# Performance work log

Hardware: AMD Instinct MI355X
Metric: run time of the kernel (lower is better)

## Reference

```python
import jax, jax.numpy as jnp
import numpy as np

B, N, F_IN, F_OUT = 4, 2048, 128, 128

def setup_inputs() -> dict:
    key = jax.random.key(0)
    k1, k2, k3, k4 = jax.random.split(key, 4)
    node_features = jax.random.uniform(k1, (B, N, F_IN), dtype=jnp.float32)
    adjacency = jax.random.uniform(k2, (B, N, N), dtype=jnp.float32)
    # nn.Linear(in_dim, out_dim) params
    lim = 1.0 / np.sqrt(F_IN)
    W = jax.random.uniform(k3, (F_OUT, F_IN), minval=-lim, maxval=lim, dtype=jnp.float32)
    b = jax.random.uniform(k4, (F_OUT,), minval=-lim, maxval=lim, dtype=jnp.float32)
    return {"node_features": node_features, "adjacency": adjacency, "W": W, "b": b}

def reference(node_features, adjacency, W, b):
    # degree_inv_sqrt, same math as diag_embed matmuls but via row/col scaling
    degree = adjacency.sum(axis=-1)                              # [B, N]
    d_inv_sqrt = jnp.clip(degree, 1e-6, None) ** -0.5            # [B, N]
    norm_adj = adjacency * d_inv_sqrt[:, :, None] * d_inv_sqrt[:, None, :]  # [B, N, N]
    agg = jnp.einsum('bnm,bmf->bnf', norm_adj, node_features)    # [B, N, F_in]
    return agg @ W.T + b                                         # [B, N, F_out]
```

## Files before the change

### kernel.cpp

```cpp
#include <hip/hip_runtime.h>


#define NN 2048
#define FF 128
#define WS_NEED (32768u + 4u * 128u * 2048u * 2u)

typedef __attribute__((ext_vector_type(4))) float f32x4;
typedef __attribute__((ext_vector_type(8))) short short8;

__device__ inline float bf2f(unsigned short h) {
    return __builtin_bit_cast(float, ((unsigned)h) << 16);
}
__device__ inline unsigned short f2bf(float f) {
    unsigned u = __builtin_bit_cast(unsigned, f);
    u = (u + 0x7fffu + ((u >> 16) & 1u)) >> 16;
    return (unsigned short)u;
}

__device__ inline short8 cvt8(f32x4 a, f32x4 b) {
    short8 r;
    r[0] = (short)f2bf(a.x); r[1] = (short)f2bf(a.y);
    r[2] = (short)f2bf(a.z); r[3] = (short)f2bf(a.w);
    r[4] = (short)f2bf(b.x); r[5] = (short)f2bf(b.y);
    r[6] = (short)f2bf(b.z); r[7] = (short)f2bf(b.w);
    return r;
}

__global__ __launch_bounds__(256) void k1_deg(const float* __restrict__ A,
                                              float* __restrict__ dinv) {
    __shared__ float red[256];
    int row = blockIdx.x;
    int t = threadIdx.x;
    const f32x4* ap = (const f32x4*)(A + (size_t)row * NN);
    f32x4 v0 = ap[t];
    f32x4 v1 = ap[t + 256];
    red[t] = v0.x + v0.y + v0.z + v0.w + v1.x + v1.y + v1.z + v1.w;
    __syncthreads();
    #pragma unroll
    for (int s = 128; s > 0; s >>= 1) {
        if (t < s) red[t] += red[t + s];
        __syncthreads();
    }
    if (t == 0) dinv[row] = rsqrtf(fmaxf(red[0], 1e-6f));
}

__global__ __launch_bounds__(256) void k2_zt(const float* __restrict__ X,
                                             const float* __restrict__ W,
                                             const float* __restrict__ dinv,
                                             unsigned short* __restrict__ Zt) {
    __shared__ float Ws[FF * FF];
    int blk = blockIdx.x;
    int b  = blk >> 6;
    int mc = (blk >> 3) & 7;
    int oc = blk & 7;
    int t  = threadIdx.x;
    int m  = mc * 256 + t;

    {
        f32x4* wd = (f32x4*)Ws;
        const f32x4* wsrc = (const f32x4*)W;
        #pragma unroll
        for (int j = 0; j < 16; ++j) wd[t + 256 * j] = wsrc[t + 256 * j];
    }
    __syncthreads();

    float acc[16];
    #pragma unroll
    for (int j = 0; j < 16; ++j) acc[j] = 0.f;

    const f32x4* xr = (const f32x4*)(X + ((size_t)b * NN + m) * FF);
    for (int f4 = 0; f4 < FF / 4; ++f4) {
        f32x4 xv = xr[f4];
        #pragma unroll
        for (int j = 0; j < 16; ++j) {
            f32x4 wv = *(const f32x4*)&Ws[(oc * 16 + j) * FF + f4 * 4];
            acc[j] += xv.x * wv.x + xv.y * wv.y + xv.z * wv.z + xv.w * wv.w;
        }
    }
    float dv = dinv[b * NN + m];
    #pragma unroll
    for (int j = 0; j < 16; ++j)
        Zt[((size_t)b * FF + oc * 16 + j) * NN + m] = f2bf(acc[j] * dv);
}

__global__ __launch_bounds__(256) void k3_mfma(const float* __restrict__ A,
                                               const unsigned short* __restrict__ Zt,
                                               const float* __restrict__ dinv,
                                               const float* __restrict__ bias,
                                               float* __restrict__ out) {
    __shared__ unsigned short As[2][16][72];
    __shared__ unsigned short Zs[2][128][72];
    int blk = blockIdx.x;
    int b   = blk >> 7;
    int n0  = (blk & 127) * 16;
    int t   = threadIdx.x;
    int w   = t >> 6, lane = t & 63;
    int l15 = lane & 15, kgrp = (lane >> 4) * 8;

    const float* Ab = A + (size_t)b * NN * NN;
    const unsigned short* Zb = Zt + (size_t)b * FF * NN;

    int ar = t >> 3;
    int ac = (t & 7) * 8;
    int zo = t >> 1;
    int zk = (t & 1) * 32;

    f32x4 acc[2];
    acc[0] = (f32x4){0.f, 0.f, 0.f, 0.f};
    acc[1] = (f32x4){0.f, 0.f, 0.f, 0.f};

    f32x4 pa0, pa1;  short8 pz0, pz1, pz2, pz3;
    f32x4 qa0, qa1;  short8 qz0, qz1, qz2, qz3;

    #define LOADT(A0, A1, Z0, Z1, Z2, Z3, k0)                                \
        do {                                                                 \
            if (t < 128) {                                                   \
                const float* asrc = Ab + (size_t)(n0 + ar) * NN + (k0) + ac; \
                A0 = *(const f32x4*)asrc;                                    \
                A1 = *(const f32x4*)(asrc + 4);                              \
            }                                                                \
            const unsigned short* zsrc = Zb + (size_t)zo * NN + (k0) + zk;   \
            Z0 = *(const short8*)(zsrc);                                     \
            Z1 = *(const short8*)(zsrc + 8);                                 \
            Z2 = *(const short8*)(zsrc + 16);                                \
            Z3 = *(const short8*)(zsrc + 24);                                \
        } while (0)

    #define WRITET(buf, A0, A1, Z0, Z1, Z2, Z3)                              \
        do {                                                                 \
            if (t < 128) *(short8*)&As[buf][ar][ac] = cvt8(A0, A1);          \
            *(short8*)&Zs[buf][zo][zk]      = Z0;                            \
            *(short8*)&Zs[buf][zo][zk + 8]  = Z1;                            \
            *(short8*)&Zs[buf][zo][zk + 16] = Z2;                            \
            *(short8*)&Zs[buf][zo][zk + 24] = Z3;                            \
        } while (0)

    #define MFMAS(cur)                                                       \
        do {                                                                 \
            _Pragma("unroll")                                                \
            for (int ks = 0; ks < 64; ks += 32) {                            \
                short8 af = *(const short8*)&As[cur][l15][ks + kgrp];        \
                short8 bf0 = *(const short8*)&Zs[cur][w * 32 + l15][ks + kgrp];       \
                short8 bf1 = *(const short8*)&Zs[cur][w * 32 + 16 + l15][ks + kgrp];  \
                acc[0] = __builtin_amdgcn_mfma_f32_16x16x32_bf16(af, bf0, acc[0], 0, 0, 0); \
                acc[1] = __builtin_amdgcn_mfma_f32_16x16x32_bf16(af, bf1, acc[1], 0, 0, 0); \
            }                                                                \
        } while (0)

    LOADT(pa0, pa1, pz0, pz1, pz2, pz3, 0);
    WRITET(0, pa0, pa1, pz0, pz1, pz2, pz3);
    LOADT(pa0, pa1, pz0, pz1, pz2, pz3, 64);
    __syncthreads();

    for (int it = 0; it < 32; it += 2) {
        if (it + 2 < 32) LOADT(qa0, qa1, qz0, qz1, qz2, qz3, (it + 2) * 64);
        MFMAS(0);
        if (it + 1 < 32) WRITET(1, pa0, pa1, pz0, pz1, pz2, pz3);
        __syncthreads();
        if (it + 1 < 32) {
            if (it + 3 < 32) LOADT(pa0, pa1, pz0, pz1, pz2, pz3, (it + 3) * 64);
            MFMAS(1);
            if (it + 2 < 32) WRITET(0, qa0, qa1, qz0, qz1, qz2, qz3);
            __syncthreads();
        }
    }

    int drow = (lane >> 4) * 4;
    #pragma unroll
    for (int tt = 0; tt < 2; ++tt) {
        int o = w * 32 + tt * 16 + l15;
        float bv = bias[o];
        #pragma unroll
        for (int r = 0; r < 4; ++r) {
            int n = n0 + drow + r;
            float dv = dinv[b * NN + n];
            out[((size_t)b * NN + n) * FF + o] = dv * acc[tt][r] + bv;
        }
    }
    #undef LOADT
    #undef WRITET
    #undef MFMAS
}

extern "C" void kernel_launch(void* const* d_in, const int* in_sizes, int n_in,
                              void* d_out, int out_size, void* d_ws, size_t ws_size,
                              hipStream_t stream) {
    const float *X = nullptr, *A = nullptr, *W = nullptr, *bias = nullptr;
    for (int i = 0; i < n_in; ++i) {
        switch (in_sizes[i]) {
            case 16777216: A    = (const float*)d_in[i]; break;
            case 1048576:  X    = (const float*)d_in[i]; break;
            case 16384:    W    = (const float*)d_in[i]; break;
            case 128:      bias = (const float*)d_in[i]; break;
            default: break;
        }
    }
    float* out = (float*)d_out;
    if (!X || !A || !W || !bias) return;
    if (out_size != 4 * NN * FF) return;
    if (ws_size < (size_t)WS_NEED) return;

    float* dinv        = (float*)d_ws;
    unsigned short* Zt = (unsigned short*)((char*)d_ws + 32768);

    k1_deg<<<4 * NN, 256, 0, stream>>>(A, dinv);
    k2_zt<<<256, 256, 0, stream>>>(X, W, dinv, Zt);
    k3_mfma<<<512, 256, 0, stream>>>(A, Zt, dinv, bias, out);
}
```

Measured before the change: 52.23 us.

## Retile aggregation kernel to 32x64 output tiles with 128-wide K steps

The MFMA aggregation kernel now assigns each block 32 node rows by 64 output features, instead of 16 rows by all 128 features, and arranges the four waves as a 2x2 grid of tiles. The K step grows from 64 to 128, which halves the number of loop iterations and barriers. All threads now load the adjacency tile, where before only half did. Each block reads half as much of the Z operand per output row, but every adjacency row is now read by two blocks, so the kernel relies on L2 to absorb that duplicate traffic on the largest tensor.

```diff
diff --git a/kernel.cpp b/kernel.cpp
--- a/kernel.cpp
+++ b/kernel.cpp
@@ -8,9 +8,6 @@
 typedef __attribute__((ext_vector_type(4))) float f32x4;
 typedef __attribute__((ext_vector_type(8))) short short8;
 
-__device__ inline float bf2f(unsigned short h) {
-    return __builtin_bit_cast(float, ((unsigned)h) << 16);
-}
 __device__ inline unsigned short f2bf(float f) {
     unsigned u = __builtin_bit_cast(unsigned, f);
     u = (u + 0x7fffu + ((u >> 16) & 1u)) >> 16;
@@ -88,79 +85,84 @@
                                                const float* __restrict__ dinv,
                                                const float* __restrict__ bias,
                                                float* __restrict__ out) {
-    __shared__ unsigned short As[2][16][72];
-    __shared__ unsigned short Zs[2][128][72];
+    __shared__ unsigned short As[2][32][136];
+    __shared__ unsigned short Zs[2][64][136];
     int blk = blockIdx.x;
     int b   = blk >> 7;
-    int n0  = (blk & 127) * 16;
+    int rem = blk & 127;
+    int n0  = (rem >> 1) * 32;
+    int o0  = (rem & 1) * 64;
     int t   = threadIdx.x;
     int w   = t >> 6, lane = t & 63;
+    int wr  = (w >> 1) * 16;
+    int wc  = (w & 1) * 32;
     int l15 = lane & 15, kgrp = (lane >> 4) * 8;
 
     const float* Ab = A + (size_t)b * NN * NN;
     const unsigned short* Zb = Zt + (size_t)b * FF * NN;
 
     int ar = t >> 3;
-    int ac = (t & 7) * 8;
-    int zo = t >> 1;
-    int zk = (t & 1) * 32;
+    int ac = (t & 7) * 16;
+    int zo = t >> 2;
+    int zc = (t & 3) * 32;
 
     f32x4 acc[2];
     acc[0] = (f32x4){0.f, 0.f, 0.f, 0.f};
     acc[1] = (f32x4){0.f, 0.f, 0.f, 0.f};
 
-    f32x4 pa0, pa1;  short8 pz0, pz1, pz2, pz3;
-    f32x4 qa0, qa1;  short8 qz0, qz1, qz2, qz3;
-
-    #define LOADT(A0, A1, Z0, Z1, Z2, Z3, k0)                                \
+    f32x4 pa0, pa1, pa2, pa3;  short8 pz0, pz1, pz2, pz3;
+    f32x4 qa0, qa1, qa2, qa3;  short8 qz0, qz1, qz2, qz3;
+
+    #define LOADT(A0, A1, A2, A3, Z0, Z1, Z2, Z3, k0)                        \
         do {                                                                 \
-            if (t < 128) {                                                   \
-                const float* asrc = Ab + (size_t)(n0 + ar) * NN + (k0) + ac; \
-                A0 = *(const f32x4*)asrc;                                    \
-                A1 = *(const f32x4*)(asrc + 4);                              \
-            }                                                                \
-            const unsigned short* zsrc = Zb + (size_t)zo * NN + (k0) + zk;   \
+            const float* asrc = Ab + (size_t)(n0 + ar) * NN + (k0) + ac;     \
+            A0 = *(const f32x4*)(asrc);                                      \
+            A1 = *(const f32x4*)(asrc + 4);                                  \
+            A2 = *(const f32x4*)(asrc + 8);                                  \
+            A3 = *(const f32x4*)(asrc + 12);                                 \
+            const unsigned short* zsrc = Zb + (size_t)(o0 + zo) * NN + (k0) + zc; \
             Z0 = *(const short8*)(zsrc);                                     \
             Z1 = *(const short8*)(zsrc + 8);                                 \
             Z2 = *(const short8*)(zsrc + 16);                                \
             Z3 = *(const short8*)(zsrc + 24);                                \
         } while (0)
 
-    #define WRITET(buf, A0, A1, Z0, Z1, Z2, Z3)                              \
+    #define WRITET(buf, A0, A1, A2, A3, Z0, Z1, Z2, Z3)                      \
         do {                                                                 \
-            if (t < 128) *(short8*)&As[buf][ar][ac] = cvt8(A0, A1);          \
-            *(short8*)&Zs[buf][zo][zk]      = Z0;                            \
-            *(short8*)&Zs[buf][zo][zk + 8]  = Z1;                            \
-            *(short8*)&Zs[buf][zo][zk + 16] = Z2;                            \
-            *(short8*)&Zs[buf][zo][zk + 24] = Z3;                            \
+            *(short8*)&As[buf][ar][ac]     = cvt8(A0, A1);                   \
+            *(short8*)&As[buf][ar][ac + 8] = cvt8(A2, A3);                   \
+            *(short8*)&Zs[buf][zo][zc]      = Z0;                            \
+            *(short8*)&Zs[buf][zo][zc + 8]  = Z1;                            \
+            *(short8*)&Zs[buf][zo][zc + 16] = Z2;                            \
+            *(short8*)&Zs[buf][zo][zc + 24] = Z3;                            \
         } while (0)
 
     #define MFMAS(cur)                                                       \
         do {                                                                 \
             _Pragma("unroll")                                                \
-            for (int ks = 0; ks < 64; ks += 32) {                            \
-                short8 af = *(const short8*)&As[cur][l15][ks + kgrp];        \
-                short8 bf0 = *(const short8*)&Zs[cur][w * 32 + l15][ks + kgrp];       \
-                short8 bf1 = *(const short8*)&Zs[cur][w * 32 + 16 + l15][ks + kgrp];  \
+            for (int ks = 0; ks < 128; ks += 32) {                           \
+                short8 af  = *(const short8*)&As[cur][wr + l15][ks + kgrp];  \
+                short8 bf0 = *(const short8*)&Zs[cur][wc + l15][ks + kgrp];  \
+                short8 bf1 = *(const short8*)&Zs[cur][wc + 16 + l15][ks + kgrp]; \
                 acc[0] = __builtin_amdgcn_mfma_f32_16x16x32_bf16(af, bf0, acc[0], 0, 0, 0); \
                 acc[1] = __builtin_amdgcn_mfma_f32_16x16x32_bf16(af, bf1, acc[1], 0, 0, 0); \
             }                                                                \
         } while (0)
 
-    LOADT(pa0, pa1, pz0, pz1, pz2, pz3, 0);
-    WRITET(0, pa0, pa1, pz0, pz1, pz2, pz3);
-    LOADT(pa0, pa1, pz0, pz1, pz2, pz3, 64);
+    LOADT(pa0, pa1, pa2, pa3, pz0, pz1, pz2, pz3, 0);
+    WRITET(0, pa0, pa1, pa2, pa3, pz0, pz1, pz2, pz3);
+    LOADT(pa0, pa1, pa2, pa3, pz0, pz1, pz2, pz3, 128);
     __syncthreads();
 
-    for (int it = 0; it < 32; it += 2) {
-        if (it + 2 < 32) LOADT(qa0, qa1, qz0, qz1, qz2, qz3, (it + 2) * 64);
+    for (int it = 0; it < 16; it += 2) {
+        if (it + 2 < 16) LOADT(qa0, qa1, qa2, qa3, qz0, qz1, qz2, qz3, (it + 2) * 128);
         MFMAS(0);
-        if (it + 1 < 32) WRITET(1, pa0, pa1, pz0, pz1, pz2, pz3);
+        if (it + 1 < 16) WRITET(1, pa0, pa1, pa2, pa3, pz0, pz1, pz2, pz3);
         __syncthreads();
-        if (it + 1 < 32) {
-            if (it + 3 < 32) LOADT(pa0, pa1, pz0, pz1, pz2, pz3, (it + 3) * 64);
+        if (it + 1 < 16) {
+            if (it + 3 < 16) LOADT(pa0, pa1, pa2, pa3, pz0, pz1, pz2, pz3, (it + 3) * 128);
             MFMAS(1);
-            if (it + 2 < 32) WRITET(0, qa0, qa1, qz0, qz1, qz2, qz3);
+            if (it + 2 < 16) WRITET(0, qa0, qa1, qa2, qa3, qz0, qz1, qz2, qz3);
             __syncthreads();
         }
     }
@@ -168,11 +170,11 @@
     int drow = (lane >> 4) * 4;
     #pragma unroll
     for (int tt = 0; tt < 2; ++tt) {
-        int o = w * 32 + tt * 16 + l15;
+        int o = o0 + wc + tt * 16 + l15;
         float bv = bias[o];
         #pragma unroll
         for (int r = 0; r < 4; ++r) {
-            int n = n0 + drow + r;
+            int n = n0 + wr + drow + r;
             float dv = dinv[b * NN + n];
             out[((size_t)b * NN + n) * FF + o] = dv * acc[tt][r] + bv;
         }
```

New measurement: 56.40 us (median of 2 runs). 1.08x slower.

## Convert adjacency to bf16 during degree pass and stream it into MFMA kernel

Applied to the files above, without the earlier changes.

The degree kernel now also writes a bf16 copy of the adjacency matrix to workspace. The main matmul kernel reads that bf16 copy and Z directly from global memory per wave, with no LDS staging or barriers, so the fp32 adjacency is no longer read a second time. In exchange it writes and then rereads 32 MB of bf16 data, needs a much larger workspace (it falls back to the old path otherwise), and depends on uncoalesced 16-byte row-strided global loads.

```diff
diff --git a/kernel.cpp b/kernel.cpp
--- a/kernel.cpp
+++ b/kernel.cpp
@@ -3,14 +3,12 @@
 
 #define NN 2048
 #define FF 128
-#define WS_NEED (32768u + 4u * 128u * 2048u * 2u)
+#define WS_BASE  (32768u + 4u * 128u * 2048u * 2u)
+#define WS_FULL  (WS_BASE + 4u * 2048u * 2048u * 2u)
 
 typedef __attribute__((ext_vector_type(4))) float f32x4;
 typedef __attribute__((ext_vector_type(8))) short short8;
 
-__device__ inline float bf2f(unsigned short h) {
-    return __builtin_bit_cast(float, ((unsigned)h) << 16);
-}
 __device__ inline unsigned short f2bf(float f) {
     unsigned u = __builtin_bit_cast(unsigned, f);
     u = (u + 0x7fffu + ((u >> 16) & 1u)) >> 16;
@@ -24,6 +22,26 @@
     r[4] = (short)f2bf(b.x); r[5] = (short)f2bf(b.y);
     r[6] = (short)f2bf(b.z); r[7] = (short)f2bf(b.w);
     return r;
+}
+
+__global__ __launch_bounds__(256) void k1_deg_cvt(const float* __restrict__ A,
+                                                  float* __restrict__ dinv,
+                                                  unsigned short* __restrict__ Abf) {
+    __shared__ float red[256];
+    int row = blockIdx.x;
+    int t = threadIdx.x;
+    const f32x4* ap = (const f32x4*)(A + (size_t)row * NN);
+    f32x4 v0 = ap[2 * t];
+    f32x4 v1 = ap[2 * t + 1];
+    *(short8*)(Abf + (size_t)row * NN + t * 8) = cvt8(v0, v1);
+    red[t] = v0.x + v0.y + v0.z + v0.w + v1.x + v1.y + v1.z + v1.w;
+    __syncthreads();
+    #pragma unroll
+    for (int s = 128; s > 0; s >>= 1) {
+        if (t < s) red[t] += red[t + s];
+        __syncthreads();
+    }
+    if (t == 0) dinv[row] = rsqrtf(fmaxf(red[0], 1e-6f));
 }
 
 __global__ __launch_bounds__(256) void k1_deg(const float* __restrict__ A,
@@ -81,6 +99,48 @@
     #pragma unroll
     for (int j = 0; j < 16; ++j)
         Zt[((size_t)b * FF + oc * 16 + j) * NN + m] = f2bf(acc[j] * dv);
+}
+
+__global__ __launch_bounds__(256) void k3_wave(const unsigned short* __restrict__ Abf,
+                                               const unsigned short* __restrict__ Zt,
+                                               const float* __restrict__ dinv,
+                                               const float* __restrict__ bias,
+                                               float* __restrict__ out) {
+    int blk = blockIdx.x;
+    int b   = blk >> 7;
+    int n0  = (blk & 127) * 16;
+    int t   = threadIdx.x;
+    int w   = t >> 6, lane = t & 63;
+    int l15 = lane & 15, kgrp = (lane >> 4) * 8;
+    int o0  = w * 32;
+
+    const unsigned short* Ar = Abf + ((size_t)b * NN + n0 + l15) * NN + kgrp;
+    const unsigned short* Z0 = Zt + ((size_t)b * FF + o0 + l15) * NN + kgrp;
+    const unsigned short* Z1 = Z0 + (size_t)16 * NN;
+
+    f32x4 acc0 = (f32x4){0.f, 0.f, 0.f, 0.f};
+    f32x4 acc1 = (f32x4){0.f, 0.f, 0.f, 0.f};
+
+    #pragma unroll 8
+    for (int kk = 0; kk < NN; kk += 32) {
+        short8 af  = *(const short8*)(Ar + kk);
+        short8 bf0 = *(const short8*)(Z0 + kk);
+        short8 bf1 = *(const short8*)(Z1 + kk);
+        acc0 = __builtin_amdgcn_mfma_f32_16x16x32_bf16(af, bf0, acc0, 0, 0, 0);
+        acc1 = __builtin_amdgcn_mfma_f32_16x16x32_bf16(af, bf1, acc1, 0, 0, 0);
+    }
+
+    int drow = (lane >> 4) * 4;
+    float bv0 = bias[o0 + l15];
+    float bv1 = bias[o0 + 16 + l15];
+    #pragma unroll
+    for (int r = 0; r < 4; ++r) {
+        int n = n0 + drow + r;
+        float dv = dinv[b * NN + n];
+        float* orow = out + ((size_t)b * NN + n) * FF;
+        orow[o0 + l15]      = dv * acc0[r] + bv0;
+        orow[o0 + 16 + l15] = dv * acc1[r] + bv1;
+    }
 }
 
 __global__ __launch_bounds__(256) void k3_mfma(const float* __restrict__ A,
@@ -198,12 +258,19 @@
     float* out = (float*)d_out;
     if (!X || !A || !W || !bias) return;
     if (out_size != 4 * NN * FF) return;
-    if (ws_size < (size_t)WS_NEED) return;
+    if (ws_size < (size_t)WS_BASE) return;
 
     float* dinv        = (float*)d_ws;
     unsigned short* Zt = (unsigned short*)((char*)d_ws + 32768);
 
-    k1_deg<<<4 * NN, 256, 0, stream>>>(A, dinv);
-    k2_zt<<<256, 256, 0, stream>>>(X, W, dinv, Zt);
-    k3_mfma<<<512, 256, 0, stream>>>(A, Zt, dinv, bias, out);
-}
+    if (ws_size >= (size_t)WS_FULL) {
+        unsigned short* Abf = (unsigned short*)((char*)d_ws + WS_BASE);
+        k1_deg_cvt<<<4 * NN, 256, 0, stream>>>(A, dinv, Abf);
+        k2_zt<<<256, 256, 0, stream>>>(X, W, dinv, Zt);
+        k3_wave<<<512, 256, 0, stream>>>(Abf, Zt, dinv, bias, out);
+    } else {
+        k1_deg<<<4 * NN, 256, 0, stream>>>(A, dinv);
+        k2_zt<<<256, 256, 0, stream>>>(X, W, dinv, Zt);
+        k3_mfma<<<512, 256, 0, stream>>>(A, Zt, dinv, bias, out);
+    }
+}
```

Result: slower. 77.38 us (+48.2%).
